# Performance work log

Measured on AMD Instinct MI355X. Metric: run time of the kernel, lower is better.

## Reference

```python
import jax, jax.numpy as jnp
import numpy as np

B, C, H, W = 4, 512, 128, 128
CQK = C // 8


def setup_inputs() -> dict:
    key = jax.random.key(0)
    ks = jax.random.split(key, 4)
    def w(k, shape, fan_in):
        return jax.random.normal(k, shape, jnp.float32) * np.float32(1.0 / np.sqrt(fan_in))
    return {
        "x": jax.random.normal(ks[0], (B, C, H, W), jnp.float32),
        "Wq": w(ks[1], (CQK, C), C), "bq": jnp.zeros((CQK,), jnp.float32),
        "Wk": w(ks[2], (CQK, C), C), "bk": jnp.zeros((CQK,), jnp.float32),
        "Wv": w(ks[3], (C, C), C), "bv": jnp.zeros((C,), jnp.float32),
    }


def _criss_cross(q, k, v):
    # q,k: [B, Cqk, H, W]; v: [B, C, H, W]
    _, _, h, w = q.shape
    # row energies: query at (y,x) vs keys (y, i) for all i -> [B, W(i), H, W]
    e_row = jnp.einsum('bchw,bchi->bihw', q, k)
    # column energies incl. self: query at (y,x) vs keys (j, x) -> [B, H(j), H, W]
    e_col = jnp.einsum('bchw,bcjw->bjhw', q, k)
    # CCNet's ca_weight excludes j == y from the column part (self term is
    # already counted once in the row part at i == x). Mask it to -inf so the
    # softmax matches the [B, H+W-1, H, W] energy exactly (masked weight = 0).
    diag = jnp.eye(h, dtype=bool)[None, :, :, None]  # [1, H(j), H(y), 1]
    e_col = jnp.where(diag, -jnp.inf, e_col)
    attn = jax.nn.softmax(jnp.concatenate([e_row, e_col], axis=1), axis=1)
    a_row, a_col = attn[:, :w], attn[:, w:]
    # ca_map: aggregate values along the same row and same column
    out = (jnp.einsum('bihw,bchi->bchw', a_row, v)
           + jnp.einsum('bjhw,bcjw->bchw', a_col, v))
    return out


def reference(x, Wq, bq, Wk, bk, Wv, bv):
    # 1x1 convs == per-pixel channel matmuls
    proj = lambda Wm, bm: jnp.einsum('bchw,oc->bohw', x, Wm) + bm[None, :, None, None]
    q = proj(Wq, bq)
    k = proj(Wk, bk)
    v = proj(Wv, bv)
    return _criss_cross(q, k, v)
```

## Files before the change

### kernel.cpp

```cpp
#include <hip/hip_runtime.h>
#include <hip/hip_bf16.h>

namespace {
constexpr int kB = 4;
constexpr int kC = 512;
constexpr int kH = 128;
constexpr int kW = 128;
constexpr int kCQK = 64;
constexpr int kL = kH * kW;
constexpr int kO = 640;

constexpr size_t OFF_WALL = 0;
constexpr size_t OFF_BALL = (size_t)kO * kC;
constexpr size_t OFF_QKV  = OFF_BALL + kO;
constexpr size_t OFF_E    = OFF_QKV + (size_t)kB * kO * kL;
constexpr size_t WS_FLOATS = OFF_E + (size_t)kB * kH * kW * 256;

typedef __attribute__((ext_vector_type(8))) short bf16x8;
typedef __attribute__((ext_vector_type(4))) float f32x4;

__device__ __forceinline__ unsigned short f32_to_bf16_rn(float f) {
  unsigned u = __float_as_uint(f);
  unsigned r = (u + 0x7FFFu + ((u >> 16) & 1u)) >> 16;
  return (unsigned short)r;
}
__device__ __forceinline__ float bf16_to_f32(unsigned short h) {
  return __uint_as_float(((unsigned)h) << 16);
}
__device__ __forceinline__ unsigned pack_bf16x2(float a, float b) {
  return (unsigned)f32_to_bf16_rn(a) | ((unsigned)f32_to_bf16_rn(b) << 16);
}
constexpr int SOW = 17;
constexpr int SOC = 16 * SOW + 1;
constexpr int ROW_SW = 132;
constexpr size_t AROWT_OFF = 2097152;
constexpr size_t QH_OFF = 0;
constexpr size_t QL_OFF = 1048576;
constexpr size_t KH_OFF = 2097152;
constexpr size_t KL_OFF = 3145728;
constexpr size_t CTMP_OFF = 8388608;
constexpr int VT_SC = 68;
constexpr int VT_SW = 16 * VT_SC + 4;
constexpr size_t VFRAG_B = (size_t)kW * 32 * 4 * 64 * 8;
}

__global__ __launch_bounds__(256) void pack_w(
    const float* __restrict__ Wq, const float* __restrict__ bq,
    const float* __restrict__ Wk, const float* __restrict__ bk,
    const float* __restrict__ Wv, const float* __restrict__ bv,
    short* __restrict__ wpk, float* __restrict__ ball) {
  const int r = blockIdx.x;
  const int t = threadIdx.x;
  const float* src;
  if (r < 64) {
    src = Wq + (size_t)r * kC;
    if (t == 0) ball[r] = bq[r];
  } else if (r < 128) {
    src = Wk + (size_t)(r - 64) * kC;
    if (t == 0) ball[r] = bk[r - 64];
  } else {
    src = Wv + (size_t)(r - 128) * kC;
    if (t == 0) ball[r] = bv[r - 128];
  }
#pragma unroll
  for (int p = 0; p < 2; ++p) {
    const int c = p * 256 + t;
    const float v = src[c];
    const unsigned short h = f32_to_bf16_rn(v);
    const unsigned short l = f32_to_bf16_rn(v - bf16_to_f32(h));
    wpk[(size_t)r * kC + c] = (short)h;
    wpk[(size_t)kO * kC + (size_t)r * kC + c] = (short)l;
  }
}

__global__ __launch_bounds__(256) void pack_x(
    const float* __restrict__ x, short* __restrict__ xpk,
    int b_off, size_t xstride) {
  __shared__ float sT[64][65];
  const int l0 = blockIdx.x * 64;
  const int c0 = blockIdx.y * 64;
  const int b = b_off + blockIdx.z;
  const int t = threadIdx.x;
  const float* xb = x + (size_t)b * kC * kL;
  short* xo = xpk + (size_t)blockIdx.z * xstride;
#pragma unroll
  for (int p = 0; p < 4; ++p) {
    const int ch = p * 256 + t;
    const int c = ch >> 4, l4 = (ch & 15) * 4;
    float4 v = *(const float4*)(xb + (size_t)(c0 + c) * kL + l0 + l4);
    sT[c][l4 + 0] = v.x; sT[c][l4 + 1] = v.y; sT[c][l4 + 2] = v.z; sT[c][l4 + 3] = v.w;
  }
  __syncthreads();
#pragma unroll
  for (int p = 0; p < 2; ++p) {
    const int ch = p * 256 + t;
    const int l = ch >> 3, cg = ch & 7;
    short hi[8], lo[8];
#pragma unroll
    for (int j = 0; j < 8; ++j) {
      const float v = sT[cg * 8 + j][l];
      const unsigned short h = f32_to_bf16_rn(v);
      hi[j] = (short)h;
      lo[j] = (short)f32_to_bf16_rn(v - bf16_to_f32(h));
    }
    short* dh = xo + (size_t)(l0 + l) * kC + c0 + cg * 8;
    *(bf16x8*)dh = *(bf16x8*)hi;
    *(bf16x8*)(dh + (size_t)kL * kC) = *(bf16x8*)lo;
  }
}

__global__ __launch_bounds__(256, 2) void proj_mfma(
    const short* __restrict__ xpk, size_t xstride,
    const short* __restrict__ wpk,
    const float* __restrict__ ball, float* __restrict__ qkv, int b_off) {
  __shared__ short A_h[128 * 64];
  __shared__ short A_l[128 * 64];
  __shared__ short B_h[128 * 64];
  __shared__ short B_l[128 * 64];
  const int mt = blockIdx.x;
  const int n0 = blockIdx.y * 128;
  const int m0 = mt * 128;
  const int b = b_off + blockIdx.z;
  const bool qk = (mt == 0);
  const int t = threadIdx.x;
  const int wid = t >> 6, lane = t & 63;
  const int wr = wid >> 1, wc = wid & 1;
  const int lr = lane & 15, lg = lane >> 4;
  const int srow8 = lane >> 3;
  const int skg = (lane & 7) ^ srow8;
  const short* xo = xpk + (size_t)blockIdx.z * xstride;

  f32x4 acc[4][4];
#pragma unroll
  for (int i = 0; i < 4; ++i)
#pragma unroll
    for (int j = 0; j < 4; ++j) acc[i][j] = (f32x4)(0.f);

  for (int kt = 0; kt < 8; ++kt) {
    const int k0 = kt * 64;
#pragma unroll
    for (int p = 0; p < 4; ++p) {
      const int ck = p * 4 + wid;
      const int row = ck * 8 + srow8;
      const short* srcA = wpk + (size_t)(m0 + row) * kC + k0 + skg * 8;
      const short* srcB = xo + (size_t)(n0 + row) * kC + k0 + skg * 8;
      __builtin_amdgcn_global_load_lds(
          (const __attribute__((address_space(1))) void*)srcA,
          (__attribute__((address_space(3))) void*)&A_h[ck * 512], 16, 0, 0);
      __builtin_amdgcn_global_load_lds(
          (const __attribute__((address_space(1))) void*)(srcA + (size_t)kO * kC),
          (__attribute__((address_space(3))) void*)&A_l[ck * 512], 16, 0, 0);
      __builtin_amdgcn_global_load_lds(
          (const __attribute__((address_space(1))) void*)srcB,
          (__attribute__((address_space(3))) void*)&B_h[ck * 512], 16, 0, 0);
      if (qk)
        __builtin_amdgcn_global_load_lds(
            (const __attribute__((address_space(1))) void*)(srcB + (size_t)kL * kC),
            (__attribute__((address_space(3))) void*)&B_l[ck * 512], 16, 0, 0);
    }
    __syncthreads();
#pragma unroll
    for (int ks = 0; ks < 2; ++ks) {
      bf16x8 ah[4], al[4], bh[4], bl[4];
#pragma unroll
      for (int mf = 0; mf < 4; ++mf) {
        const int row = wr * 64 + mf * 16 + lr;
        const int kg = ks * 4 + lg;
        const int off = row * 64 + ((kg ^ (row & 7)) << 3);
        ah[mf] = *(const bf16x8*)&A_h[off];
        al[mf] = *(const bf16x8*)&A_l[off];
      }
#pragma unroll
      for (int nf = 0; nf < 4; ++nf) {
        const int row = wc * 64 + nf * 16 + lr;
        const int kg = ks * 4 + lg;
        const int off = row * 64 + ((kg ^ (row & 7)) << 3);
        bh[nf] = *(const bf16x8*)&B_h[off];
        if (qk) bl[nf] = *(const bf16x8*)&B_l[off];
      }
#pragma unroll
      for (int mf = 0; mf < 4; ++mf)
#pragma unroll
        for (int nf = 0; nf < 4; ++nf) {
          acc[mf][nf] = __builtin_amdgcn_mfma_f32_16x16x32_bf16(
              ah[mf], bh[nf], acc[mf][nf], 0, 0, 0);
          acc[mf][nf] = __builtin_amdgcn_mfma_f32_16x16x32_bf16(
              al[mf], bh[nf], acc[mf][nf], 0, 0, 0);
          if (qk)
            acc[mf][nf] = __builtin_amdgcn_mfma_f32_16x16x32_bf16(
                ah[mf], bl[nf], acc[mf][nf], 0, 0, 0);
        }
    }
    __syncthreads();
  }
  if (qk) {
    unsigned short* qw = (unsigned short*)qkv + (size_t)b * kO * kL * 2
        + (wr ? KH_OFF : QH_OFF);
    unsigned short* tb = (unsigned short*)(qkv + ((size_t)b * kO + 128) * kL)
        + CTMP_OFF + (wr ? 2097152 : 0);
#pragma unroll
    for (int mf = 0; mf < 4; ++mf) {
      const int c0 = mf * 16 + lg * 4;
#pragma unroll
      for (int nf = 0; nf < 4; ++nf) {
        const int l = n0 + wc * 64 + nf * 16 + lr;
        unsigned short hi4[4], lo4[4];
#pragma unroll
        for (int r = 0; r < 4; ++r) {
          const float val = acc[mf][nf][r] + ball[wr * 64 + c0 + r];
          const unsigned short h = f32_to_bf16_rn(val);
          hi4[r] = h;
          lo4[r] = f32_to_bf16_rn(val - bf16_to_f32(h));
        }
        unsigned short* d = qw + ((size_t)l * 64 + c0);
        *(uint2*)d = *(uint2*)hi4;
        *(uint2*)(d + QL_OFF) = *(uint2*)lo4;
        const int hh = l >> 7, ww = l & 127;
        unsigned short* dT = tb + (((size_t)ww * 128 + hh) * 64 + c0);
        *(uint2*)dT = *(uint2*)hi4;
        *(uint2*)(dT + 1048576) = *(uint2*)lo4;
      }
    }
  } else {
    unsigned short* vbf =
        (unsigned short*)(qkv + ((size_t)b * kO + 128) * kL);
#pragma unroll
    for (int mf = 0; mf < 4; ++mf) {
#pragma unroll
      for (int r = 0; r < 4; ++r) {
        const int m = m0 + wr * 64 + mf * 16 + lg * 4 + r;
        const float bias = ball[m];
        unsigned short* dst = vbf + (size_t)(m - 128) * kL + n0 + wc * 64;
#pragma unroll
        for (int nf = 0; nf < 4; ++nf) {
          dst[nf * 16 + lr] = f32_to_bf16_rn(acc[mf][nf][r] + bias);
        }
      }
    }
  }
}

template <int COL>
__global__ __launch_bounds__(256) void escore_mfma(
    const unsigned short* __restrict__ qh, const unsigned short* __restrict__ ql,
    const unsigned short* __restrict__ kh, const unsigned short* __restrict__ kl,
    float* __restrict__ e) {
  const int bi = blockIdx.x;
  const int b = bi >> 7, idx = bi & 127;
  const int t = threadIdx.x;
  const int wid = t >> 6, lane = t & 63;
  const int wj = wid >> 1, wh = wid & 1;
  const int lr = lane & 15, lg = lane >> 4;

  const size_t base = (size_t)b * ((size_t)kO * kL * 2) + (size_t)idx * 8192;

  f32x4 acc[4][4];
#pragma unroll
  for (int i = 0; i < 4; ++i)
#pragma unroll
    for (int j = 0; j < 4; ++j) acc[i][j] = (f32x4)(0.f);

#pragma unroll
  for (int ks = 0; ks < 2; ++ks) {
    bf16x8 ah[4], al[4], bh[4], bl[4];
#pragma unroll
    for (int mf = 0; mf < 4; ++mf) {
      const size_t ro = base + (size_t)(wj * 64 + mf * 16 + lr) * 64
          + ks * 32 + lg * 8;
      ah[mf] = *(const bf16x8*)(kh + ro);
      al[mf] = *(const bf16x8*)(kl + ro);
    }
#pragma unroll
    for (int nf = 0; nf < 4; ++nf) {
      const size_t ro = base + (size_t)(wh * 64 + nf * 16 + lr) * 64
          + ks * 32 + lg * 8;
      bh[nf] = *(const bf16x8*)(qh + ro);
      bl[nf] = *(const bf16x8*)(ql + ro);
    }
#pragma unroll
    for (int mf = 0; mf < 4; ++mf)
#pragma unroll
      for (int nf = 0; nf < 4; ++nf) {
        acc[mf][nf] = __builtin_amdgcn_mfma_f32_16x16x32_bf16(
            ah[mf], bh[nf], acc[mf][nf], 0, 0, 0);
        acc[mf][nf] = __builtin_amdgcn_mfma_f32_16x16x32_bf16(
            ah[mf], bl[nf], acc[mf][nf], 0, 0, 0);
        acc[mf][nf] = __builtin_amdgcn_mfma_f32_16x16x32_bf16(
            al[mf], bh[nf], acc[mf][nf], 0, 0, 0);
      }
  }
  const float NEG_INF = __int_as_float(0xff800000);
#pragma unroll
  for (int mf = 0; mf < 4; ++mf) {
    const int row0 = wj * 64 + mf * 16 + lg * 4;
#pragma unroll
    for (int nf = 0; nf < 4; ++nf) {
      const int cl = wh * 64 + nf * 16 + lr;
      float o[4];
#pragma unroll
      for (int r = 0; r < 4; ++r) {
        float v = acc[mf][nf][r];
        if (COL && (row0 + r == cl)) v = NEG_INF;
        o[r] = v;
      }
      float* dst;
      if (COL)
        dst = e + (((size_t)b * kH + cl) * kW + idx) * 256 + 128 + row0;
      else
        dst = e + (((size_t)b * kH + idx) * kW + cl) * 256 + row0;
      *(float4*)dst = *(const float4*)o;
    }
  }
}

__global__ __launch_bounds__(256) void softmax_kernel(
    float* __restrict__ e, float* qkv_base) {
  const int t = threadIdx.x;
  const int wv = t >> 6, lane = t & 63;
  const size_t pix = (size_t)blockIdx.x * 4 + wv;
  float* p = e + pix * 256 + lane * 4;
  float4 v = *(const float4*)p;
  float m = fmaxf(fmaxf(v.x, v.y), fmaxf(v.z, v.w));
#pragma unroll
  for (int off = 32; off > 0; off >>= 1) m = fmaxf(m, __shfl_xor(m, off, 64));
  float e0 = expf(v.x - m), e1 = expf(v.y - m), e2 = expf(v.z - m), e3 = expf(v.w - m);
  float s = e0 + e1 + e2 + e3;
#pragma unroll
  for (int off = 32; off > 0; off >>= 1) s += __shfl_xor(s, off, 64);
  const float inv = 1.0f / s;
  const float o0 = e0 * inv, o1 = e1 * inv, o2 = e2 * inv, o3 = e3 * inv;
  const int b = (int)(pix >> 14);
  const int h = (int)((pix >> 7) & 127);
  const int w = (int)(pix & 127);
  unsigned short* base = (unsigned short*)qkv_base + (size_t)b * kO * kL * 2;
  if (lane < 32) {
    unsigned short* dst = base + AROWT_OFF + (((size_t)h * kW + w) * 128 + lane * 4);
    *(uint2*)dst = make_uint2(pack_bf16x2(o0, o1), pack_bf16x2(o2, o3));
  } else {
    const int s32 = lane - 32;
    const int jb = s32 >> 3;
    const int lg = (s32 >> 1) & 3;
    const int eoff = (s32 & 1) * 4;
    const int hb = h >> 4, hr = h & 15;
    unsigned short* dst = base + (size_t)w * 16384
        + (((size_t)(jb * 8 + hb) * 64 + lg * 16 + hr) * 8 + eoff);
    *(uint2*)dst = make_uint2(pack_bf16x2(o0, o1), pack_bf16x2(o2, o3));
  }
}

__global__ __launch_bounds__(256) void vtrans_kernel(
    const float* __restrict__ qkv, unsigned short* __restrict__ vfrag) {
  __shared__ float sT[16 * VT_SW];
  const int cb = blockIdx.x;
  const int wt = blockIdx.y;
  const int b  = blockIdx.z;
  const int t = threadIdx.x;
  const int lane = t & 63, wd = t >> 6;
  const int lr = lane & 15, lg = lane >> 4;
  const unsigned short* vb =
      (const unsigned short*)(qkv + ((size_t)b * kO + 128) * kL)
      + (size_t)(cb * 16) * kL + wt * 16;
  unsigned short* vfb = vfrag + (size_t)b * VFRAG_B;

  for (int half = 0; half < 2; ++half) {
    const int j0 = half * 64;
#pragma unroll
    for (int p = 0; p < 16; ++p) {
      const int g = p * 256 + t;
      const int wq = g & 3;
      const int j = (g >> 2) & 63;
      const int ci = p;
      uint2 v2 = *(const uint2*)(vb + (size_t)ci * kL + (size_t)(j0 + j) * kW + wq * 4);
      float* d = sT + ci * VT_SC + j;
      d[(wq * 4 + 0) * VT_SW] = bf16_to_f32((unsigned short)(v2.x & 0xffff));
      d[(wq * 4 + 1) * VT_SW] = bf16_to_f32((unsigned short)(v2.x >> 16));
      d[(wq * 4 + 2) * VT_SW] = bf16_to_f32((unsigned short)(v2.y & 0xffff));
      d[(wq * 4 + 3) * VT_SW] = bf16_to_f32((unsigned short)(v2.y >> 16));
    }
    __syncthreads();
#pragma unroll
    for (int wi = 0; wi < 4; ++wi) {
      const int w = wd * 4 + wi;
#pragma unroll
      for (int ktl = 0; ktl < 2; ++ktl) {
        const float* s = sT + w * VT_SW + lr * VT_SC + ktl * 32 + lg * 8;
        float a[8];
        *(float4*)(a + 0) = *(const float4*)(s + 0);
        *(float4*)(a + 4) = *(const float4*)(s + 4);
        const int ktg = half * 2 + ktl;
        unsigned short* dst = vfb
            + ((((size_t)(wt * 16 + w) * 32 + cb) * 4 + ktg) * 64 + lane) * 8;
        uint4 o = make_uint4(pack_bf16x2(a[0], a[1]), pack_bf16x2(a[2], a[3]),
                             pack_bf16x2(a[4], a[5]), pack_bf16x2(a[6], a[7]));
        *(uint4*)dst = o;
      }
    }
    __syncthreads();
  }
}

__global__ __launch_bounds__(1024) void colagg_mfma(
    float* qkv, const unsigned short* __restrict__ vfrag) {
  __shared__ float sO[64 * SOC];
  const int gx = blockIdx.x;
  const int ct = gx & 7, ht = gx >> 3;
  const int c0 = ct * 64, h0 = ht * 64;
  const int w0 = blockIdx.y * 16;
  const int b = blockIdx.z;
  const int t = threadIdx.x;
  const int wv = t >> 6, lane = t & 63;
  const int lr = lane & 15, lg = lane >> 4;
  const int w = w0 + wv;

  f32x4 acc[4][4];
#pragma unroll
  for (int i = 0; i < 4; ++i)
#pragma unroll
    for (int j = 0; j < 4; ++j) acc[i][j] = (f32x4)(0.f);

  const unsigned short* ab = (const unsigned short*)qkv + (size_t)b * kO * kL * 2
      + (size_t)w * 16384;
  const unsigned short* vfb = vfrag + (size_t)b * VFRAG_B
      + ((size_t)w * 32 + ct * 4) * 2048;
  unsigned short* ctmp =
      (unsigned short*)(qkv + ((size_t)b * kO + 128) * kL) + CTMP_OFF;

  for (int kt = 0; kt < 4; ++kt) {
    bf16x8 vf[4], af[4];
#pragma unroll
    for (int mf = 0; mf < 4; ++mf)
      vf[mf] = *(const bf16x8*)(vfb + ((size_t)mf * 2048 + kt * 512 + lane * 8));
#pragma unroll
    for (int nf = 0; nf < 4; ++nf)
      af[nf] = *(const bf16x8*)(
          ab + (((size_t)(kt * 8 + ht * 4 + nf) * 64 + lane) * 8));
#pragma unroll
    for (int mf = 0; mf < 4; ++mf)
#pragma unroll
      for (int nf = 0; nf < 4; ++nf)
        acc[mf][nf] = __builtin_amdgcn_mfma_f32_16x16x32_bf16(
            vf[mf], af[nf], acc[mf][nf], 0, 0, 0);
  }

  const int ew4 = t & 3, ehh = (t >> 2) & 15, ecb = t >> 6;
  for (int nf = 0; nf < 4; ++nf) {
    __syncthreads();
#pragma unroll
    for (int mf = 0; mf < 4; ++mf)
#pragma unroll
      for (int r = 0; r < 4; ++r)
        sO[(mf * 16 + lg * 4 + r) * SOC + lr * SOW + wv] = acc[mf][nf][r];
    __syncthreads();
#pragma unroll
    for (int q = 0; q < 4; ++q) {
      const int c = q * 16 + ecb;
      const float* s = &sO[c * SOC + ehh * SOW + ew4 * 4];
      unsigned u0 = pack_bf16x2(s[0], s[1]);
      unsigned u1 = pack_bf16x2(s[2], s[3]);
      unsigned short* dst = ctmp + ((size_t)(c0 + c) * kL
          + (size_t)(h0 + nf * 16 + ehh) * kW + w0 + ew4 * 4);
      *(uint2*)dst = make_uint2(u0, u1);
    }
  }
}

__global__ __launch_bounds__(256) void rowagg_mfma(
    const float* qkv, float* __restrict__ out) {
  __shared__ float sO[64 * ROW_SW];
  const int ct = blockIdx.x;
  const int bh = blockIdx.y;
  const int b = bh >> 7, h = bh & 127;
  const int c0 = ct * 128;
  const int t = threadIdx.x;
  const int wid = t >> 6, lane = t & 63;
  const int wr = wid >> 1, wc = wid & 1;
  const int lr = lane & 15, lg = lane >> 4;

  f32x4 acc[4][4];
#pragma unroll
  for (int i = 0; i < 4; ++i)
#pragma unroll
    for (int j = 0; j < 4; ++j) acc[i][j] = (f32x4)(0.f);

  const unsigned short* vbf =
      (const unsigned short*)(qkv + ((size_t)b * kO + 128) * kL);
  const unsigned short* ctmp = vbf + CTMP_OFF;
  const unsigned short* arbase = (const unsigned short*)qkv
      + (size_t)b * kO * kL * 2 + AROWT_OFF + (size_t)h * kW * 128;

#pragma unroll
  for (int s = 0; s < 4; ++s) {
    bf16x8 vfr[4], afr[4];
#pragma unroll
    for (int mf = 0; mf < 4; ++mf) {
      const int c = c0 + wr * 64 + mf * 16 + lr;
      vfr[mf] = *(const bf16x8*)(
          vbf + (size_t)c * kL + (size_t)h * kW + s * 32 + lg * 8);
    }
#pragma unroll
    for (int nf = 0; nf < 4; ++nf) {
      const int w = wc * 64 + nf * 16 + lr;
      afr[nf] = *(const bf16x8*)(arbase + (size_t)w * 128 + s * 32 + lg * 8);
    }
#pragma unroll
    for (int mf = 0; mf < 4; ++mf)
#pragma unroll
      for (int nf = 0; nf < 4; ++nf)
        acc[mf][nf] = __builtin_amdgcn_mfma_f32_16x16x32_bf16(
            vfr[mf], afr[nf], acc[mf][nf], 0, 0, 0);
  }

  const int wq = t & 31;
  const int cc8 = t >> 5;
  const unsigned short* ctb = ctmp + (size_t)h * kW;
  float* outb = out + ((size_t)b * kC * kL + (size_t)h * kW);
  for (int half = 0; half < 2; ++half) {
    if (wr == half) {
#pragma unroll
      for (int mf = 0; mf < 4; ++mf)
#pragma unroll
        for (int nf = 0; nf < 4; ++nf)
#pragma unroll
          for (int r = 0; r < 4; ++r)
            sO[(mf * 16 + lg * 4 + r) * ROW_SW + wc * 64 + nf * 16 + lr] =
                acc[mf][nf][r];
    }
    __syncthreads();
#pragma unroll
    for (int i = 0; i < 8; ++i) {
      const int cl = i * 8 + cc8;
      const size_t c = c0 + half * 64 + cl;
      float4 v = *(const float4*)&sO[cl * ROW_SW + wq * 4];
      uint2 c2 = *(const uint2*)(ctb + c * kL + wq * 4);
      v.x += bf16_to_f32((unsigned short)(c2.x & 0xffff));
      v.y += bf16_to_f32((unsigned short)(c2.x >> 16));
      v.z += bf16_to_f32((unsigned short)(c2.y & 0xffff));
      v.w += bf16_to_f32((unsigned short)(c2.y >> 16));
      *(float4*)(outb + c * kL + wq * 4) = v;
    }
    __syncthreads();
  }
}

extern "C" void kernel_launch(void* const* d_in, const int* in_sizes, int n_in,
                              void* d_out, int out_size, void* d_ws, size_t ws_size,
                              hipStream_t stream) {
  (void)in_sizes; (void)n_in; (void)out_size;
  const float* x  = (const float*)d_in[0];
  const float* Wq = (const float*)d_in[1];
  const float* bq = (const float*)d_in[2];
  const float* Wk = (const float*)d_in[3];
  const float* bk = (const float*)d_in[4];
  const float* Wv = (const float*)d_in[5];
  const float* bv = (const float*)d_in[6];
  float* out = (float*)d_out;
  float* ws  = (float*)d_ws;

  short* wpk = (short*)(ws + OFF_WALL);
  float* ball = ws + OFF_BALL;
  float* qkv  = ws + OFF_QKV;
  float* e    = ws + OFF_E;
  unsigned short* vfrag = (unsigned short*)(ws + OFF_E);

  pack_w<<<dim3(kO), dim3(256), 0, stream>>>(Wq, bq, Wk, bk, Wv, bv, wpk, ball);

  const size_t xpk_batch = (size_t)2 * kL * kC;
  const size_t need = WS_FLOATS * sizeof(float)
      + (size_t)kB * xpk_batch * sizeof(short);
  if (ws_size >= need) {
    short* xall = (short*)(ws + WS_FLOATS);
    pack_x<<<dim3(kL / 64, kC / 64, kB), dim3(256), 0, stream>>>(
        x, xall, 0, xpk_batch);
    proj_mfma<<<dim3(5, kL / 128, kB), dim3(256), 0, stream>>>(
        xall, xpk_batch, wpk, ball, qkv, 0);
  } else {
    short* xpk = (short*)(ws + OFF_E);
    for (int b = 0; b < kB; ++b) {
      pack_x<<<dim3(kL / 64, kC / 64, 1), dim3(256), 0, stream>>>(x, xpk, b, 0);
      proj_mfma<<<dim3(5, kL / 128, 1), dim3(256), 0, stream>>>(
          xpk, 0, wpk, ball, qkv, b);
    }
  }

  unsigned short* qkb0 = (unsigned short*)qkv;
  escore_mfma<0><<<dim3(kB * kH), dim3(256), 0, stream>>>(
      qkb0 + QH_OFF, qkb0 + QL_OFF, qkb0 + KH_OFF, qkb0 + KL_OFF, e);
  unsigned short* vt0 = (unsigned short*)qkv + (size_t)128 * kL * 2 + CTMP_OFF;
  escore_mfma<1><<<dim3(kB * kW), dim3(256), 0, stream>>>(
      vt0 + 0, vt0 + 1048576, vt0 + 2097152, vt0 + 3145728, e);
  softmax_kernel<<<dim3(kB * kH * kW / 4), dim3(256), 0, stream>>>(e, qkv);
  vtrans_kernel<<<dim3(32, 8, kB), dim3(256), 0, stream>>>(qkv, vfrag);
  colagg_mfma<<<dim3(16, kW / 16, kB), dim3(1024), 0, stream>>>(qkv, vfrag);
  rowagg_mfma<<<dim3(4, kB * kH), dim3(256), 0, stream>>>(qkv, out);
}
```

Measured before the change: 397.9 us.

## Stage projection epilogue through LDS, remap blocks per XCD, split QK transpose

The projection epilogue now writes its results into swizzled shared memory and then issues coalesced 16-byte global stores, in place of scattered 8-byte and 2-byte writes. The strided transposed Q/K copy is taken out of the projection kernel and done by a separate qktrans kernel. The grid is flattened to 1D with an XCD-aware mapping so that the five M-tiles sharing one x tile land on the same XCD and can reuse it in L2. The cost is an extra kernel launch, an extra read and write pass over Q/K, and a larger LDS footprint that may affect occupancy.

```diff
diff --git a/kernel.cpp b/kernel.cpp
--- a/kernel.cpp
+++ b/kernel.cpp
@@ -6,7 +6,6 @@
 constexpr int kC = 512;
 constexpr int kH = 128;
 constexpr int kW = 128;
-constexpr int kCQK = 64;
 constexpr int kL = kH * kW;
 constexpr int kO = 640;
 
@@ -112,23 +111,33 @@
 __global__ __launch_bounds__(256, 2) void proj_mfma(
     const short* __restrict__ xpk, size_t xstride,
     const short* __restrict__ wpk,
-    const float* __restrict__ ball, float* __restrict__ qkv, int b_off) {
-  __shared__ short A_h[128 * 64];
-  __shared__ short A_l[128 * 64];
-  __shared__ short B_h[128 * 64];
-  __shared__ short B_l[128 * 64];
-  const int mt = blockIdx.x;
-  const int n0 = blockIdx.y * 128;
+    const float* __restrict__ ball, float* __restrict__ qkv,
+    int b_off, int gpx) {
+  __shared__ short S[34816];
+  short* A_h = S;
+  short* A_l = S + 8192;
+  short* B_h = S + 16384;
+  short* B_l = S + 24576;
+
+  const int L = blockIdx.x;
+  const int xcd = L & 7;
+  const int s = L >> 3;
+  const int q5 = s / 5;
+  const int mt = s - q5 * 5;
+  const int g = xcd * gpx + q5;
+  const int zz = g >> 7;
+  const int b = b_off + zz;
+  const int n0 = (g & 127) * 128;
   const int m0 = mt * 128;
-  const int b = b_off + blockIdx.z;
   const bool qk = (mt == 0);
+
   const int t = threadIdx.x;
   const int wid = t >> 6, lane = t & 63;
   const int wr = wid >> 1, wc = wid & 1;
   const int lr = lane & 15, lg = lane >> 4;
   const int srow8 = lane >> 3;
   const int skg = (lane & 7) ^ srow8;
-  const short* xo = xpk + (size_t)blockIdx.z * xstride;
+  const short* xo = xpk + (size_t)zz * xstride;
 
   f32x4 acc[4][4];
 #pragma unroll
@@ -193,49 +202,92 @@
     }
     __syncthreads();
   }
+
   if (qk) {
-    unsigned short* qw = (unsigned short*)qkv + (size_t)b * kO * kL * 2
-        + (wr ? KH_OFF : QH_OFF);
-    unsigned short* tb = (unsigned short*)(qkv + ((size_t)b * kO + 128) * kL)
-        + CTMP_OFF + (wr ? 2097152 : 0);
+    short* sHI = S;
+    short* sLO = S + 17408;
 #pragma unroll
     for (int mf = 0; mf < 4; ++mf) {
-      const int c0 = mf * 16 + lg * 4;
-#pragma unroll
-      for (int nf = 0; nf < 4; ++nf) {
-        const int l = n0 + wc * 64 + nf * 16 + lr;
-        unsigned short hi4[4], lo4[4];
-#pragma unroll
-        for (int r = 0; r < 4; ++r) {
-          const float val = acc[mf][nf][r] + ball[wr * 64 + c0 + r];
+#pragma unroll
+      for (int r = 0; r < 4; ++r) {
+        const int m = wr * 64 + mf * 16 + lg * 4 + r;
+        const float bias = ball[m];
+#pragma unroll
+        for (int nf = 0; nf < 4; ++nf) {
+          const int lo_l = wc * 64 + nf * 16 + lr;
+          const float val = acc[mf][nf][r] + bias;
           const unsigned short h = f32_to_bf16_rn(val);
-          hi4[r] = h;
-          lo4[r] = f32_to_bf16_rn(val - bf16_to_f32(h));
+          const unsigned short lo = f32_to_bf16_rn(val - bf16_to_f32(h));
+          const int addr = lo_l * 136 + (((m >> 3) ^ (lo_l & 7)) << 3) + (m & 7);
+          sHI[addr] = (short)h;
+          sLO[addr] = (short)lo;
         }
-        unsigned short* d = qw + ((size_t)l * 64 + c0);
-        *(uint2*)d = *(uint2*)hi4;
-        *(uint2*)(d + QL_OFF) = *(uint2*)lo4;
-        const int hh = l >> 7, ww = l & 127;
-        unsigned short* dT = tb + (((size_t)ww * 128 + hh) * 64 + c0);
-        *(uint2*)dT = *(uint2*)hi4;
-        *(uint2*)(dT + 1048576) = *(uint2*)lo4;
       }
     }
+    __syncthreads();
+    unsigned short* qkbb = (unsigned short*)qkv + (size_t)b * kO * kL * 2;
+#pragma unroll
+    for (int it = 0; it < 8; ++it) {
+      const int tt = it * 256 + t;
+      const int ch = tt & 7;
+      const int plane = (tt >> 3) & 1;
+      const int lo_l = tt >> 4;
+      const int phys = plane * 8 + (ch ^ (lo_l & 7));
+      uint4 h4 = *(const uint4*)&sHI[lo_l * 136 + phys * 8];
+      uint4 l4 = *(const uint4*)&sLO[lo_l * 136 + phys * 8];
+      unsigned short* qw = qkbb + (plane ? KH_OFF : QH_OFF)
+          + ((size_t)(n0 + lo_l) * 64 + ch * 8);
+      *(uint4*)qw = h4;
+      *(uint4*)(qw + QL_OFF) = l4;
+    }
   } else {
+    short* sV16 = S;
+#pragma unroll
+    for (int mf = 0; mf < 4; ++mf) {
+#pragma unroll
+      for (int r = 0; r < 4; ++r) {
+        const int m = wr * 64 + mf * 16 + lg * 4 + r;
+        const float bias = ball[m0 + m];
+#pragma unroll
+        for (int nf = 0; nf < 4; ++nf) {
+          const int lo_l = wc * 64 + nf * 16 + lr;
+          const int addr = m * 136 + ((((lo_l) >> 3) ^ (m & 7)) << 3) + (lo_l & 7);
+          sV16[addr] = (short)f32_to_bf16_rn(acc[mf][nf][r] + bias);
+        }
+      }
+    }
+    __syncthreads();
     unsigned short* vbf =
         (unsigned short*)(qkv + ((size_t)b * kO + 128) * kL);
 #pragma unroll
-    for (int mf = 0; mf < 4; ++mf) {
-#pragma unroll
-      for (int r = 0; r < 4; ++r) {
-        const int m = m0 + wr * 64 + mf * 16 + lg * 4 + r;
-        const float bias = ball[m];
-        unsigned short* dst = vbf + (size_t)(m - 128) * kL + n0 + wc * 64;
-#pragma unroll
-        for (int nf = 0; nf < 4; ++nf) {
-          dst[nf * 16 + lr] = f32_to_bf16_rn(acc[mf][nf][r] + bias);
-        }
-      }
+    for (int it = 0; it < 8; ++it) {
+      const int tt = it * 256 + t;
+      const int ch = tt & 15;
+      const int m = tt >> 4;
+      const int phys = ch ^ (m & 7);
+      uint4 v4 = *(const uint4*)&sV16[m * 136 + phys * 8];
+      *(uint4*)(vbf + (size_t)(m0 + m - 128) * kL + n0 + ch * 8) = v4;
+    }
+  }
+}
+
+__global__ __launch_bounds__(256) void qktrans_kernel(float* qkv) {
+  const int h = blockIdx.x;
+  const int b = blockIdx.y;
+  const unsigned short* qkb = (const unsigned short*)qkv + (size_t)b * kO * kL * 2;
+  unsigned short* tb =
+      (unsigned short*)(qkv + ((size_t)b * kO + 128) * kL) + CTMP_OFF;
+  const int t = threadIdx.x;
+  const int q8 = t & 7, wbase = t >> 3;
+#pragma unroll
+  for (int plane = 0; plane < 4; ++plane) {
+    const unsigned short* src = qkb + (size_t)plane * 1048576;
+    unsigned short* dst = tb + (size_t)plane * 1048576;
+#pragma unroll
+    for (int ps = 0; ps < 4; ++ps) {
+      const int w = wbase + ps * 32;
+      uint4 v = *(const uint4*)(src + ((size_t)h * 128 + w) * 64 + q8 * 8);
+      *(uint4*)(dst + ((size_t)w * 128 + h) * 64 + q8 * 8) = v;
     }
   }
 }
@@ -571,16 +623,18 @@
     short* xall = (short*)(ws + WS_FLOATS);
     pack_x<<<dim3(kL / 64, kC / 64, kB), dim3(256), 0, stream>>>(
         x, xall, 0, xpk_batch);
-    proj_mfma<<<dim3(5, kL / 128, kB), dim3(256), 0, stream>>>(
-        xall, xpk_batch, wpk, ball, qkv, 0);
+    proj_mfma<<<dim3(2560), dim3(256), 0, stream>>>(
+        xall, xpk_batch, wpk, ball, qkv, 0, 64);
   } else {
     short* xpk = (short*)(ws + OFF_E);
     for (int b = 0; b < kB; ++b) {
       pack_x<<<dim3(kL / 64, kC / 64, 1), dim3(256), 0, stream>>>(x, xpk, b, 0);
-      proj_mfma<<<dim3(5, kL / 128, 1), dim3(256), 0, stream>>>(
-          xpk, 0, wpk, ball, qkv, b);
-    }
-  }
+      proj_mfma<<<dim3(640), dim3(256), 0, stream>>>(
+          xpk, 0, wpk, ball, qkv, b, 16);
+    }
+  }
+
+  qktrans_kernel<<<dim3(kH, kB), dim3(256), 0, stream>>>(qkv);
 
   unsigned short* qkb0 = (unsigned short*)qkv;
   escore_mfma<0><<<dim3(kB * kH), dim3(256), 0, stream>>>(
```

Result: no change. 394.0 us (-1.0%).
